# Kernel tuning notes

Measured on AMD Instinct MI355X. Metric: run time of the kernel, lower is better.

## Reference

```python
import jax, jax.numpy as jnp
import numpy as np

HEAD_SIZE = 64
BLOCK_SIZE = 4096
BATCH = 4


def setup_inputs() -> dict:
    key = jax.random.key(0)
    kx, kk, kq, kv = jax.random.split(key, 4)
    x = jax.random.normal(kx, (BATCH, BLOCK_SIZE, HEAD_SIZE), dtype=jnp.float32)
    s = HEAD_SIZE ** -0.5  # ~ torch default linear init scale
    Wk = jax.random.uniform(kk, (HEAD_SIZE, HEAD_SIZE), jnp.float32, -s, s)
    Wq = jax.random.uniform(kq, (HEAD_SIZE, HEAD_SIZE), jnp.float32, -s, s)
    Wv = jax.random.uniform(kv, (HEAD_SIZE, HEAD_SIZE), jnp.float32, -s, s)
    return {"x": x, "Wk": Wk, "Wq": Wq, "Wv": Wv}


def reference(x, Wk, Wq, Wv):
    # x: [B, T, C]; W*: [C, C] stored torch-style (out, in) -> y = x @ W.T
    B, T, C = x.shape
    k = x @ Wk.T  # [B, T, C]
    q = x @ Wq.T
    v = x @ Wv.T
    scores = jnp.einsum('btc,bsc->bts', q, k) * (C ** -0.5)  # [B, T, T]
    causal = jnp.tril(jnp.ones((T, T), dtype=bool))
    scores = jnp.where(causal, scores, -jnp.inf)
    weights = jax.nn.softmax(scores, axis=-1)
    out = jnp.einsum('bts,bsc->btc', weights, v)  # [B, T, C]
    return out
```

## Files before the change

### kernel.cpp

```cpp
#include <hip/hip_runtime.h>
#include <hip/hip_bf16.h>

typedef unsigned short u16;
typedef unsigned int u32;
typedef __bf16 bf16x8_t __attribute__((ext_vector_type(8)));
typedef float f32x4_t __attribute__((ext_vector_type(4)));

constexpr int Bb = 4;
constexpr int Tt = 4096;
constexpr int Dd = 64;
constexpr float QSCALE = 0.18033688011112042f;

__device__ __forceinline__ u16 f2bf(float f) {
  unsigned int u = __builtin_bit_cast(unsigned int, f);
  return (u16)((u + 0x7fffu + ((u >> 16) & 1u)) >> 16);
}
__device__ __forceinline__ u32 pk2(float a, float b) {
  return (u32)f2bf(a) | ((u32)f2bf(b) << 16);
}
__device__ __forceinline__ bf16x8_t ld16(const u16* p) {
  int4 v = *(const int4*)p;
  return __builtin_bit_cast(bf16x8_t, v);
}
__device__ __forceinline__ f32x4_t mfma16(bf16x8_t a, bf16x8_t b, f32x4_t c) {
  return __builtin_amdgcn_mfma_f32_16x16x32_bf16(a, b, c, 0, 0, 0);
}

__global__ __launch_bounds__(256) void HeadV1_proj(
    const float* __restrict__ x, const float* __restrict__ Wk,
    const float* __restrict__ Wq, const float* __restrict__ Wv,
    u16* __restrict__ qS, u16* __restrict__ kS, u16* __restrict__ vS)
{
  __shared__ u16 xl[64][72];
  __shared__ u16 Wl[3][64][72];
  __shared__ u16 ylds[64][72];

  const int t = threadIdx.x;
  const int w = t >> 6, lane = t & 63, l15 = lane & 15, quad = lane >> 4;
  const int r0 = blockIdx.x * 64;
  const int b  = r0 >> 12;
  const int kt = (r0 & 4095) >> 6;
  const long tilebase = ((long)(b * 64 + kt)) * 4096;

  {
    const float* srcs[4] = {x + (long)r0 * 64, Wk, Wq, Wv};
    u16* dstl[4] = {&xl[0][0], &Wl[0][0][0], &Wl[1][0][0], &Wl[2][0][0]};
    #pragma unroll
    for (int mm = 0; mm < 4; mm++) {
      const float* s = srcs[mm];
      u16* d = dstl[mm];
      #pragma unroll
      for (int i = 0; i < 4; i++) {
        const int f4 = i * 256 + t;
        const int row = f4 >> 4, c4 = f4 & 15;
        float4 v = ((const float4*)(s + row * 64))[c4];
        uint2 pk;
        pk.x = pk2(v.x, v.y);
        pk.y = pk2(v.z, v.w);
        *(uint2*)(d + row * 72 + c4 * 4) = pk;
      }
    }
  }
  __syncthreads();

  bf16x8_t xf[2];
  #pragma unroll
  for (int kh = 0; kh < 2; kh++)
    xf[kh] = ld16(&xl[w * 16 + l15][kh * 32 + quad * 8]);

  u16* dsts[3];
  dsts[0] = kS + tilebase; dsts[1] = qS + tilebase; dsts[2] = vS + tilebase;

  #pragma unroll
  for (int m = 0; m < 3; m++) {
    float vals[4][4];
    #pragma unroll
    for (int g = 0; g < 4; g++) {
      f32x4_t acc = {0.f, 0.f, 0.f, 0.f};
      #pragma unroll
      for (int kh = 0; kh < 2; kh++) {
        bf16x8_t wf = ld16(&Wl[m][g * 16 + l15][kh * 32 + quad * 8]);
        acc = mfma16(xf[kh], wf, acc);
      }
      #pragma unroll
      for (int r = 0; r < 4; r++)
        vals[g][r] = (m == 1) ? acc[r] * QSCALE : acc[r];
    }
    #pragma unroll
    for (int g = 0; g < 4; g++)
      #pragma unroll
      for (int r = 0; r < 4; r++)
        ylds[w * 16 + quad * 4 + r][g * 16 + l15] = f2bf(vals[g][r]);
    __syncthreads();
    if (m < 2) {
      #pragma unroll
      for (int kk = 0; kk < 2; kk++) {
        bf16x8_t f = ld16(&ylds[w * 16 + l15][kk * 32 + quad * 8]);
        *(int4*)(dsts[m] + (w * 2 + kk) * 512 + lane * 8) = __builtin_bit_cast(int4, f);
      }
    } else {
      #pragma unroll
      for (int kk = 0; kk < 2; kk++) {
        u16 tmp[8];
        #pragma unroll
        for (int j = 0; j < 8; j++)
          tmp[j] = ylds[kk * 32 + quad * 8 + j][w * 16 + l15];
        *(int4*)(dsts[2] + (kk * 4 + w) * 512 + lane * 8) = *(const int4*)tmp;
      }
    }
    __syncthreads();
  }
}

__global__ __launch_bounds__(1024, 4) void HeadV1_flash(
    const u16* __restrict__ qS, const u16* __restrict__ kS,
    const u16* __restrict__ vS, float* __restrict__ outg)
{
  __shared__ __align__(16) char smem[81920];
  u16  (*pT)[2][32][36] = (u16 (*)[2][32][36])smem;
  float (*chk)[16][33]  = (float (*)[16][33])smem;
  float (*stg)[32][68]  = (float (*)[32][68])(smem + 33792);
  float (*lst)[4][32]   = (float (*)[4][32])(smem + 73728);

  const int t    = threadIdx.x;
  const int w    = t >> 6;
  const int lane = t & 63;
  const int l15  = lane & 15;
  const int quad = lane >> 4;

  const int b  = blockIdx.x & 3;
  const int i  = blockIdx.x >> 2;
  const int j1 = i, j2 = 127 - i;
  const int nk1 = (j1 >> 1) + 1;
  const int nk2 = (j2 >> 1) + 1;
  int n1 = (16 * nk1 + 32) / 65;
  if (n1 < 1) n1 = 1;
  if (n1 > 15) n1 = 15;

  const bool grp2 = (w >= n1);
  const int j   = grp2 ? j2 : j1;
  const int nk  = grp2 ? nk2 : nk1;
  const int str = grp2 ? (16 - n1) : n1;
  const int off = grp2 ? (w - n1) : w;

  const int qt64 = j >> 1;
  const int ql0  = (j & 1) * 32;
  const int qr0  = j * 32;
  const long base = (long)b * Tt * Dd;

  const f32x4_t zero4 = {0.f, 0.f, 0.f, 0.f};

  const u16* qtile = qS + ((long)(b * 64 + qt64)) * 4096 + lane * 8;
  bf16x8_t qfrag[2][2];
  #pragma unroll
  for (int ct = 0; ct < 2; ct++)
    #pragma unroll
    for (int kd = 0; kd < 2; kd++)
      qfrag[ct][kd] = ld16(qtile + ((ql0 / 16 + ct) * 2 + kd) * 512);

  f32x4_t O[4][2];
  #pragma unroll
  for (int a = 0; a < 4; a++)
    #pragma unroll
    for (int c = 0; c < 2; c++)
      O[a][c] = zero4;
  float Lp[2] = {0.f, 0.f};

  const u16* kb = kS + ((long)(b * 64)) * 4096 + lane * 8;
  const u16* vb = vS + ((long)(b * 64)) * 4096 + lane * 8;

  auto Astage = [&](int kt_, int kk_, int par_, const bf16x8_t* kf) {
    const bool ismask = (kt_ == nk - 1);
    const int kv0 = kt_ * 64;
    #pragma unroll
    for (int rtl = 0; rtl < 2; rtl++) {
      const int rt = kk_ * 2 + rtl;
      #pragma unroll
      for (int ct = 0; ct < 2; ct++) {
        f32x4_t acc = zero4;
        acc = mfma16(kf[2 * rtl + 0], qfrag[ct][0], acc);
        acc = mfma16(kf[2 * rtl + 1], qfrag[ct][1], acc);
        if (ismask) {
          const int kvl = kv0 + rt * 16 + quad * 4;
          const int qi  = qr0 + ct * 16 + l15;
          #pragma unroll
          for (int r = 0; r < 4; r++)
            if (kvl + r > qi) acc[r] = -1e30f;
        }
        const float p0 = __builtin_amdgcn_exp2f(acc[0]);
        const float p1 = __builtin_amdgcn_exp2f(acc[1]);
        const float p2 = __builtin_amdgcn_exp2f(acc[2]);
        const float p3 = __builtin_amdgcn_exp2f(acc[3]);
        const u32 u0 = __builtin_bit_cast(u32, p0);
        const u32 u1 = __builtin_bit_cast(u32, p1);
        const u32 u2 = __builtin_bit_cast(u32, p2);
        const u32 u3 = __builtin_bit_cast(u32, p3);
        const u32 h1 = u1 & 0xFFFF0000u, h3 = u3 & 0xFFFF0000u;
        const float q0 = __builtin_bit_cast(float, u0 & 0xFFFF0000u);
        const float q1 = __builtin_bit_cast(float, h1);
        const float q2 = __builtin_bit_cast(float, u2 & 0xFFFF0000u);
        const float q3 = __builtin_bit_cast(float, h3);
        Lp[ct] += (q0 + q1) + (q2 + q3);
        uint2 pk;
        pk.x = (u0 >> 16) | h1;
        pk.y = (u2 >> 16) | h3;
        *(uint2*)&pT[w][par_][ct * 16 + l15][rtl * 16 + quad * 4] = pk;
      }
    }
  };

  auto Bstage = [&](int par_, const bf16x8_t* vf) {
    bf16x8_t pf0 = ld16(&pT[w][par_][l15][quad * 8]);
    bf16x8_t pf1 = ld16(&pT[w][par_][16 + l15][quad * 8]);
    __builtin_amdgcn_s_setprio(1);
    #pragma unroll
    for (int dt = 0; dt < 4; dt++) {
      O[dt][0] = mfma16(vf[dt], pf0, O[dt][0]);
      O[dt][1] = mfma16(vf[dt], pf1, O[dt][1]);
    }
    __builtin_amdgcn_s_setprio(0);
  };

  const int nv  = (nk - 1 - off) / str + 1;
  const int nph = 2 * nv;

  bf16x8_t vfC[4];
  {
    const u16* kt_ = kb + (long)off * 4096;
    const u16* vt_ = vb + (long)off * 4096;
    bf16x8_t kfT[4];
    #pragma unroll
    for (int f = 0; f < 4; f++) { kfT[f] = ld16(kt_ + f * 512); vfC[f] = ld16(vt_ + f * 512); }
    Astage(off, 0, 0, kfT);
  }
  int par = 0;

  for (int ph = 1; ph < nph; ph++) {
    const int ktP = off + (ph >> 1) * str;
    const int kkP = ph & 1;
    const u16* kt_ = kb + (long)ktP * 4096 + kkP * 2048;
    const u16* vt_ = vb + (long)ktP * 4096 + kkP * 2048;
    bf16x8_t kfT[4], vfN[4];
    #pragma unroll
    for (int f = 0; f < 4; f++) { kfT[f] = ld16(kt_ + f * 512); vfN[f] = ld16(vt_ + f * 512); }
    Bstage(par, vfC);
    Astage(ktP, kkP, par ^ 1, kfT);
    #pragma unroll
    for (int f = 0; f < 4; f++) vfC[f] = vfN[f];
    par ^= 1;
  }
  Bstage(par, vfC);

  lst[w][quad][l15]      = Lp[0];
  lst[w][quad][16 + l15] = Lp[1];
  __syncthreads();

  #pragma unroll
  for (int dt = 0; dt < 4; dt++) {
    #pragma unroll
    for (int ct = 0; ct < 2; ct++)
      #pragma unroll
      for (int r = 0; r < 4; r++)
        chk[w][quad * 4 + r][ct * 16 + l15] = O[dt][ct][r];
    __syncthreads();
    {
      const int jsel = t >> 9, tt = t & 511;
      const int d2 = tt >> 5, q = tt & 31;
      const int lo = jsel ? n1 : 0, hi = jsel ? 16 : n1;
      float s = 0.f;
      for (int w2 = lo; w2 < hi; w2++) s += chk[w2][d2][q];
      stg[jsel][q][dt * 16 + d2] = s;
    }
    __syncthreads();
  }

  {
    const int jsel = t >> 9, tt = t & 511;
    const int q = tt >> 4, dg = tt & 15;
    const int lo = jsel ? n1 : 0, hi = jsel ? 16 : n1;
    float L = 0.f;
    for (int w2 = lo; w2 < hi; w2++) {
      #pragma unroll
      for (int qd = 0; qd < 4; qd++) L += lst[w2][qd][q];
    }
    const float invL = 1.0f / L;
    const int jj = jsel ? j2 : j1;
    float4 v = *(const float4*)&stg[jsel][q][dg * 4];
    v.x *= invL; v.y *= invL; v.z *= invL; v.w *= invL;
    *(float4*)(outg + base + (long)(jj * 32 + q) * 64 + dg * 4) = v;
  }
}

extern "C" void kernel_launch(void* const* d_in, const int* in_sizes, int n_in,
                              void* d_out, int out_size, void* d_ws, size_t ws_size,
                              hipStream_t stream) {
  (void)in_sizes; (void)n_in; (void)out_size; (void)ws_size;
  const float* x  = (const float*)d_in[0];
  const float* Wk = (const float*)d_in[1];
  const float* Wq = (const float*)d_in[2];
  const float* Wv = (const float*)d_in[3];
  float* out = (float*)d_out;
  u16* qw  = (u16*)d_ws;
  u16* kw  = qw + (size_t)Bb * Tt * Dd;
  u16* vw  = kw + (size_t)Bb * Tt * Dd;

  HeadV1_proj<<<(Bb * Tt) / 64, 256, 0, stream>>>(x, Wk, Wq, Wv, qw, kw, vw);
  HeadV1_flash<<<256, 1024, 0, stream>>>(qw, kw, vw, out);
}
```

Baseline: 85.89 us.

## Split flash attention into 64-row query tiles with KV halves and combine kernel

Restructures the attention kernel so each block uses 512 threads and handles 64-query tiles. Each block processes a paired short and long tile in sequence, covering half of the causal KV range for each. Partial O and L sums go to workspace, and a new small kernel adds the two halves and normalizes. The aim is better load balance and more query reuse per K/V load, at the cost of an extra launch, global round-trips for the partials, and more registers per wave.

```diff
diff --git a/kernel.cpp b/kernel.cpp
--- a/kernel.cpp
+++ b/kernel.cpp
@@ -112,15 +112,16 @@
   }
 }
 
-__global__ __launch_bounds__(1024, 4) void HeadV1_flash(
+__global__ __launch_bounds__(512, 2) void HeadV1_flash(
     const u16* __restrict__ qS, const u16* __restrict__ kS,
-    const u16* __restrict__ vS, float* __restrict__ outg)
+    const u16* __restrict__ vS, float* __restrict__ Opart,
+    float* __restrict__ Lpart)
 {
   __shared__ __align__(16) char smem[81920];
-  u16  (*pT)[2][32][36] = (u16 (*)[2][32][36])smem;
-  float (*chk)[16][33]  = (float (*)[16][33])smem;
-  float (*stg)[32][68]  = (float (*)[32][68])(smem + 33792);
-  float (*lst)[4][32]   = (float (*)[4][32])(smem + 73728);
+  u16  (*pT)[2][64][36] = (u16 (*)[2][64][36])smem;
+  float (*chk)[16][66]  = (float (*)[16][66])smem;
+  float (*stg)[68]      = (float (*)[68])(smem + 33792);
+  float (*lst)[4][64]   = (float (*)[4][64])(smem + 73728);
 
   const int t    = threadIdx.x;
   const int w    = t >> 6;
@@ -128,166 +129,195 @@
   const int l15  = lane & 15;
   const int quad = lane >> 4;
 
-  const int b  = blockIdx.x & 3;
-  const int i  = blockIdx.x >> 2;
-  const int j1 = i, j2 = 127 - i;
-  const int nk1 = (j1 >> 1) + 1;
-  const int nk2 = (j2 >> 1) + 1;
-  int n1 = (16 * nk1 + 32) / 65;
-  if (n1 < 1) n1 = 1;
-  if (n1 > 15) n1 = 15;
-
-  const bool grp2 = (w >= n1);
-  const int j   = grp2 ? j2 : j1;
-  const int nk  = grp2 ? nk2 : nk1;
-  const int str = grp2 ? (16 - n1) : n1;
-  const int off = grp2 ? (w - n1) : w;
-
-  const int qt64 = j >> 1;
-  const int ql0  = (j & 1) * 32;
-  const int qr0  = j * 32;
-  const long base = (long)b * Tt * Dd;
+  const int b = blockIdx.x & 3;
+  const int s = blockIdx.x >> 2;
+  const int p = s >> 1;
+  const int h = s & 1;
 
   const f32x4_t zero4 = {0.f, 0.f, 0.f, 0.f};
-
-  const u16* qtile = qS + ((long)(b * 64 + qt64)) * 4096 + lane * 8;
-  bf16x8_t qfrag[2][2];
-  #pragma unroll
-  for (int ct = 0; ct < 2; ct++)
-    #pragma unroll
-    for (int kd = 0; kd < 2; kd++)
-      qfrag[ct][kd] = ld16(qtile + ((ql0 / 16 + ct) * 2 + kd) * 512);
-
-  f32x4_t O[4][2];
-  #pragma unroll
-  for (int a = 0; a < 4; a++)
-    #pragma unroll
-    for (int c = 0; c < 2; c++)
-      O[a][c] = zero4;
-  float Lp[2] = {0.f, 0.f};
-
   const u16* kb = kS + ((long)(b * 64)) * 4096 + lane * 8;
   const u16* vb = vS + ((long)(b * 64)) * 4096 + lane * 8;
 
-  auto Astage = [&](int kt_, int kk_, int par_, const bf16x8_t* kf) {
-    const bool ismask = (kt_ == nk - 1);
-    const int kv0 = kt_ * 64;
-    #pragma unroll
-    for (int rtl = 0; rtl < 2; rtl++) {
-      const int rt = kk_ * 2 + rtl;
-      #pragma unroll
-      for (int ct = 0; ct < 2; ct++) {
-        f32x4_t acc = zero4;
-        acc = mfma16(kf[2 * rtl + 0], qfrag[ct][0], acc);
-        acc = mfma16(kf[2 * rtl + 1], qfrag[ct][1], acc);
-        if (ismask) {
-          const int kvl = kv0 + rt * 16 + quad * 4;
-          const int qi  = qr0 + ct * 16 + l15;
+  #pragma unroll 1
+  for (int tau = 0; tau < 2; tau++) {
+    const int i   = tau ? (63 - p) : p;
+    const int nk  = i + 1;
+    const int mid = (nk + 1) >> 1;
+    const int lo  = h ? mid : 0;
+    const int hi  = h ? nk : mid;
+    const int qr0 = i * 64;
+
+    bf16x8_t qfrag[4][2];
+    {
+      const u16* qtile = qS + ((long)(b * 64 + i)) * 4096 + lane * 8;
+      #pragma unroll
+      for (int ct = 0; ct < 4; ct++)
+        #pragma unroll
+        for (int kd = 0; kd < 2; kd++)
+          qfrag[ct][kd] = ld16(qtile + (ct * 2 + kd) * 512);
+    }
+
+    f32x4_t O[4][4];
+    #pragma unroll
+    for (int a = 0; a < 4; a++)
+      #pragma unroll
+      for (int c = 0; c < 4; c++)
+        O[a][c] = zero4;
+    float Lp[4] = {0.f, 0.f, 0.f, 0.f};
+
+    auto Astage = [&](int kt_, int kk_, int par_, const bf16x8_t* kf) {
+      const bool ismask = (kt_ == nk - 1);
+      const int kv0 = kt_ * 64;
+      #pragma unroll
+      for (int rtl = 0; rtl < 2; rtl++) {
+        const int rt = kk_ * 2 + rtl;
+        #pragma unroll
+        for (int ct = 0; ct < 4; ct++) {
+          f32x4_t acc = zero4;
+          acc = mfma16(kf[2 * rtl + 0], qfrag[ct][0], acc);
+          acc = mfma16(kf[2 * rtl + 1], qfrag[ct][1], acc);
+          if (ismask) {
+            const int kvl = kv0 + rt * 16 + quad * 4;
+            const int qi  = qr0 + ct * 16 + l15;
+            #pragma unroll
+            for (int r = 0; r < 4; r++)
+              if (kvl + r > qi) acc[r] = -1e30f;
+          }
+          const float p0 = __builtin_amdgcn_exp2f(acc[0]);
+          const float p1 = __builtin_amdgcn_exp2f(acc[1]);
+          const float p2 = __builtin_amdgcn_exp2f(acc[2]);
+          const float p3 = __builtin_amdgcn_exp2f(acc[3]);
+          const u32 u0 = __builtin_bit_cast(u32, p0);
+          const u32 u1 = __builtin_bit_cast(u32, p1);
+          const u32 u2 = __builtin_bit_cast(u32, p2);
+          const u32 u3 = __builtin_bit_cast(u32, p3);
+          const u32 h1 = u1 & 0xFFFF0000u, h3 = u3 & 0xFFFF0000u;
+          const float q0 = __builtin_bit_cast(float, u0 & 0xFFFF0000u);
+          const float q1 = __builtin_bit_cast(float, h1);
+          const float q2 = __builtin_bit_cast(float, u2 & 0xFFFF0000u);
+          const float q3 = __builtin_bit_cast(float, h3);
+          Lp[ct] += (q0 + q1) + (q2 + q3);
+          uint2 pk;
+          pk.x = (u0 >> 16) | h1;
+          pk.y = (u2 >> 16) | h3;
+          *(uint2*)&pT[w][par_][ct * 16 + l15][rtl * 16 + quad * 4] = pk;
+        }
+      }
+    };
+
+    auto Bstage = [&](int par_, const bf16x8_t* vf) {
+      bf16x8_t pf[4];
+      #pragma unroll
+      for (int ct = 0; ct < 4; ct++)
+        pf[ct] = ld16(&pT[w][par_][ct * 16 + l15][quad * 8]);
+      __builtin_amdgcn_s_setprio(1);
+      #pragma unroll
+      for (int dt = 0; dt < 4; dt++)
+        #pragma unroll
+        for (int ct = 0; ct < 4; ct++)
+          O[dt][ct] = mfma16(vf[dt], pf[ct], O[dt][ct]);
+      __builtin_amdgcn_s_setprio(0);
+    };
+
+    const int span = hi - lo;
+    const int nv = (w < span) ? ((span - 1 - w) / 8 + 1) : 0;
+
+    if (nv > 0) {
+      bf16x8_t vfC[4];
+      int par = 0;
+      {
+        const u16* kt_ = kb + (long)(lo + w) * 4096;
+        const u16* vt_ = vb + (long)(lo + w) * 4096;
+        bf16x8_t kfT[4];
+        #pragma unroll
+        for (int f = 0; f < 4; f++) { kfT[f] = ld16(kt_ + f * 512); vfC[f] = ld16(vt_ + f * 512); }
+        Astage(lo + w, 0, 0, kfT);
+      }
+      const int nph = 2 * nv;
+      for (int ph = 1; ph < nph; ph++) {
+        const int ktP = lo + w + (ph >> 1) * 8;
+        const int kkP = ph & 1;
+        const u16* kt_ = kb + (long)ktP * 4096 + kkP * 2048;
+        const u16* vt_ = vb + (long)ktP * 4096 + kkP * 2048;
+        bf16x8_t kfT[4], vfN[4];
+        #pragma unroll
+        for (int f = 0; f < 4; f++) { kfT[f] = ld16(kt_ + f * 512); vfN[f] = ld16(vt_ + f * 512); }
+        Bstage(par, vfC);
+        Astage(ktP, kkP, par ^ 1, kfT);
+        #pragma unroll
+        for (int f = 0; f < 4; f++) vfC[f] = vfN[f];
+        par ^= 1;
+      }
+      Bstage(par, vfC);
+    }
+
+    #pragma unroll
+    for (int ct = 0; ct < 4; ct++)
+      lst[w][quad][ct * 16 + l15] = Lp[ct];
+    __syncthreads();
+
+    #pragma unroll
+    for (int dt = 0; dt < 4; dt++) {
+      #pragma unroll
+      for (int ct = 0; ct < 4; ct++)
+        #pragma unroll
+        for (int r = 0; r < 4; r++)
+          chk[w][quad * 4 + r][ct * 16 + l15] = O[dt][ct][r];
+      __syncthreads();
+      #pragma unroll
+      for (int rep = 0; rep < 2; rep++) {
+        const int cell = rep * 512 + t;
+        const int d2 = cell >> 6, q = cell & 63;
+        float sacc = 0.f;
+        #pragma unroll
+        for (int w2 = 0; w2 < 8; w2++) sacc += chk[w2][d2][q];
+        stg[q][dt * 16 + d2] = sacc;
+      }
+      __syncthreads();
+    }
+
+    {
+      float* Od = Opart + ((long)(b * 64 + i)) * 8192 + (long)h * 4096;
+      #pragma unroll
+      for (int rep = 0; rep < 2; rep++) {
+        const int idx = rep * 512 + t;
+        const int q = idx >> 4, dg = idx & 15;
+        *(f32x4_t*)(Od + q * 64 + dg * 4) = *(const f32x4_t*)&stg[q][dg * 4];
+      }
+      if (t < 64) {
+        float L = 0.f;
+        #pragma unroll
+        for (int w2 = 0; w2 < 8; w2++)
           #pragma unroll
-          for (int r = 0; r < 4; r++)
-            if (kvl + r > qi) acc[r] = -1e30f;
-        }
-        const float p0 = __builtin_amdgcn_exp2f(acc[0]);
-        const float p1 = __builtin_amdgcn_exp2f(acc[1]);
-        const float p2 = __builtin_amdgcn_exp2f(acc[2]);
-        const float p3 = __builtin_amdgcn_exp2f(acc[3]);
-        const u32 u0 = __builtin_bit_cast(u32, p0);
-        const u32 u1 = __builtin_bit_cast(u32, p1);
-        const u32 u2 = __builtin_bit_cast(u32, p2);
-        const u32 u3 = __builtin_bit_cast(u32, p3);
-        const u32 h1 = u1 & 0xFFFF0000u, h3 = u3 & 0xFFFF0000u;
-        const float q0 = __builtin_bit_cast(float, u0 & 0xFFFF0000u);
-        const float q1 = __builtin_bit_cast(float, h1);
-        const float q2 = __builtin_bit_cast(float, u2 & 0xFFFF0000u);
-        const float q3 = __builtin_bit_cast(float, h3);
-        Lp[ct] += (q0 + q1) + (q2 + q3);
-        uint2 pk;
-        pk.x = (u0 >> 16) | h1;
-        pk.y = (u2 >> 16) | h3;
-        *(uint2*)&pT[w][par_][ct * 16 + l15][rtl * 16 + quad * 4] = pk;
-      }
-    }
-  };
-
-  auto Bstage = [&](int par_, const bf16x8_t* vf) {
-    bf16x8_t pf0 = ld16(&pT[w][par_][l15][quad * 8]);
-    bf16x8_t pf1 = ld16(&pT[w][par_][16 + l15][quad * 8]);
-    __builtin_amdgcn_s_setprio(1);
-    #pragma unroll
-    for (int dt = 0; dt < 4; dt++) {
-      O[dt][0] = mfma16(vf[dt], pf0, O[dt][0]);
-      O[dt][1] = mfma16(vf[dt], pf1, O[dt][1]);
-    }
-    __builtin_amdgcn_s_setprio(0);
-  };
-
-  const int nv  = (nk - 1 - off) / str + 1;
-  const int nph = 2 * nv;
-
-  bf16x8_t vfC[4];
-  {
-    const u16* kt_ = kb + (long)off * 4096;
-    const u16* vt_ = vb + (long)off * 4096;
-    bf16x8_t kfT[4];
-    #pragma unroll
-    for (int f = 0; f < 4; f++) { kfT[f] = ld16(kt_ + f * 512); vfC[f] = ld16(vt_ + f * 512); }
-    Astage(off, 0, 0, kfT);
-  }
-  int par = 0;
-
-  for (int ph = 1; ph < nph; ph++) {
-    const int ktP = off + (ph >> 1) * str;
-    const int kkP = ph & 1;
-    const u16* kt_ = kb + (long)ktP * 4096 + kkP * 2048;
-    const u16* vt_ = vb + (long)ktP * 4096 + kkP * 2048;
-    bf16x8_t kfT[4], vfN[4];
-    #pragma unroll
-    for (int f = 0; f < 4; f++) { kfT[f] = ld16(kt_ + f * 512); vfN[f] = ld16(vt_ + f * 512); }
-    Bstage(par, vfC);
-    Astage(ktP, kkP, par ^ 1, kfT);
-    #pragma unroll
-    for (int f = 0; f < 4; f++) vfC[f] = vfN[f];
-    par ^= 1;
-  }
-  Bstage(par, vfC);
-
-  lst[w][quad][l15]      = Lp[0];
-  lst[w][quad][16 + l15] = Lp[1];
-  __syncthreads();
-
-  #pragma unroll
-  for (int dt = 0; dt < 4; dt++) {
-    #pragma unroll
-    for (int ct = 0; ct < 2; ct++)
-      #pragma unroll
-      for (int r = 0; r < 4; r++)
-        chk[w][quad * 4 + r][ct * 16 + l15] = O[dt][ct][r];
-    __syncthreads();
-    {
-      const int jsel = t >> 9, tt = t & 511;
-      const int d2 = tt >> 5, q = tt & 31;
-      const int lo = jsel ? n1 : 0, hi = jsel ? 16 : n1;
-      float s = 0.f;
-      for (int w2 = lo; w2 < hi; w2++) s += chk[w2][d2][q];
-      stg[jsel][q][dt * 16 + d2] = s;
+          for (int qd = 0; qd < 4; qd++) L += lst[w2][qd][t];
+        Lpart[((long)(b * 64 + i)) * 128 + h * 64 + t] = L;
+      }
     }
     __syncthreads();
   }
-
-  {
-    const int jsel = t >> 9, tt = t & 511;
-    const int q = tt >> 4, dg = tt & 15;
-    const int lo = jsel ? n1 : 0, hi = jsel ? 16 : n1;
-    float L = 0.f;
-    for (int w2 = lo; w2 < hi; w2++) {
-      #pragma unroll
-      for (int qd = 0; qd < 4; qd++) L += lst[w2][qd][q];
-    }
-    const float invL = 1.0f / L;
-    const int jj = jsel ? j2 : j1;
-    float4 v = *(const float4*)&stg[jsel][q][dg * 4];
-    v.x *= invL; v.y *= invL; v.z *= invL; v.w *= invL;
-    *(float4*)(outg + base + (long)(jj * 32 + q) * 64 + dg * 4) = v;
+}
+
+__global__ __launch_bounds__(256) void HeadV1_out(
+    const float* __restrict__ Opart, const float* __restrict__ Lpart,
+    float* __restrict__ outg)
+{
+  __shared__ float Ls[64];
+  const int t = threadIdx.x;
+  const int tile = blockIdx.x;
+  const int b = tile >> 6, i = tile & 63;
+  const float* O0 = Opart + (long)tile * 8192;
+  const float* O1 = O0 + 4096;
+  if (t < 64) Ls[t] = Lpart[(long)tile * 128 + t] + Lpart[(long)tile * 128 + 64 + t];
+  __syncthreads();
+  #pragma unroll
+  for (int r = 0; r < 4; r++) {
+    const int idx = r * 256 + t;
+    const int q = idx >> 4, c4 = idx & 15;
+    f32x4_t v = *(const f32x4_t*)(O0 + q * 64 + c4 * 4);
+    v += *(const f32x4_t*)(O1 + q * 64 + c4 * 4);
+    const float invL = 1.0f / Ls[q];
+    v *= invL;
+    *(f32x4_t*)(outg + ((long)b * Tt + (long)(i * 64 + q)) * 64 + c4 * 4) = v;
   }
 }
 
@@ -300,10 +330,13 @@
   const float* Wq = (const float*)d_in[2];
   const float* Wv = (const float*)d_in[3];
   float* out = (float*)d_out;
-  u16* qw  = (u16*)d_ws;
-  u16* kw  = qw + (size_t)Bb * Tt * Dd;
-  u16* vw  = kw + (size_t)Bb * Tt * Dd;
+  u16* qw = (u16*)d_ws;
+  u16* kw = qw + (size_t)Bb * Tt * Dd;
+  u16* vw = kw + (size_t)Bb * Tt * Dd;
+  float* Op = (float*)(vw + (size_t)Bb * Tt * Dd);
+  float* Lp = Op + (size_t)(Bb * 64) * 8192;
 
   HeadV1_proj<<<(Bb * Tt) / 64, 256, 0, stream>>>(x, Wk, Wq, Wv, qw, kw, vw);
-  HeadV1_flash<<<256, 1024, 0, stream>>>(qw, kw, vw, out);
-}
+  HeadV1_flash<<<256, 512, 0, stream>>>(qw, kw, vw, Op, Lp);
+  HeadV1_out<<<Bb * 64, 256, 0, stream>>>(Op, Lp, out);
+}
```

New measurement: 95.23 us. 10.9% more time.
